# Kernel tuning notes

Hardware: AMD Instinct MI355X
Metric: run time of the kernel (lower is better)

Reference implementation:

```python
import math
import jax, jax.numpy as jnp
import numpy as np

B, T, M, S, D, H = 16, 512, 8, 32, 256, 4
HD = D // H


def setup_inputs() -> dict:
    key = jax.random.key(0)
    ks = jax.random.split(key, 16)
    w = 1.0 / math.sqrt(D)
    return {
        'q_temporal': jax.random.normal(ks[0], (B, T, M, D), jnp.float32),
        'q_static': jax.random.normal(ks[1], (B, S, D), jnp.float32),
        'k_temporal': jax.random.normal(ks[2], (B, T, M, D), jnp.float32),
        'v_temporal': jax.random.normal(ks[3], (B, T, M, D), jnp.float32),
        'k_static': jax.random.normal(ks[4], (B, S, D), jnp.float32),
        'v_static': jax.random.normal(ks[5], (B, S, D), jnp.float32),
        'q_w': jax.random.normal(ks[6], (D, D), jnp.float32) * w,
        'q_b': jax.random.normal(ks[7], (D,), jnp.float32) * w,
        'k_w': jax.random.normal(ks[8], (D, D), jnp.float32) * w,
        'k_b': jax.random.normal(ks[9], (D,), jnp.float32) * w,
        'v_w': jax.random.normal(ks[10], (D, D), jnp.float32) * w,
        'v_b': jax.random.normal(ks[11], (D,), jnp.float32) * w,
        'o_w': jax.random.normal(ks[12], (D, D), jnp.float32) * w,
        'o_b': jax.random.normal(ks[13], (D,), jnp.float32) * w,
        'mask_temporal': jax.random.randint(ks[14], (B, T, M), 0, 2).astype(jnp.int32),
        'mask_fcst': jax.random.randint(ks[15], (B, T, M), 0, 2).astype(jnp.int32),
        'mask_static': jnp.ones((B, S), jnp.int32),
    }


def _lin(x, w, b):
    # torch.nn.Linear: y = x @ W^T + b
    return x @ w.T + b


def reference(q_temporal, q_static, k_temporal, v_temporal, k_static, v_static,
              q_w, q_b, k_w, k_b, v_w, v_b, o_w, o_b,
              mask_temporal, mask_fcst, mask_static):
    scale = 1.0 / math.sqrt(HD)

    def heads5(x):  # [B,T,M,D] -> [B,H,T,M,HD]
        return x.reshape(B, T, M, H, HD).transpose(0, 3, 1, 2, 4)

    def heads3(x):  # [B,S,D] -> [B,H,S,HD]
        return x.reshape(B, -1, H, HD).transpose(0, 2, 1, 3)

    Qt = heads5(_lin(q_temporal, q_w, q_b))
    Kt = heads5(_lin(k_temporal, k_w, k_b))
    Vt = heads5(_lin(v_temporal, v_w, v_b))
    Qs = heads3(_lin(q_static, q_w, q_b))
    Ks = heads3(_lin(k_static, k_w, k_b))
    Vs = heads3(_lin(v_static, v_w, v_b))

    # additive masks: 0 where valid (==1), -inf where padded
    mt = jnp.where(mask_temporal == 1, 0.0, -jnp.inf).astype(Qt.dtype)  # [B,T,M]
    ms = jnp.where(mask_static == 1, 0.0, -jnp.inf).astype(Qt.dtype)    # [B,S]

    # ---- temporal query branch ----
    # temp_temp: per-timestep modality-vs-modality attention, column key mask
    Qt_Kt = jnp.einsum('bhtmd,bhtnd->bhtmn', Qt, Kt) * scale + mt[:, None, :, None, :]
    # temp_static: temporal queries vs static keys
    Qt_Ks = jnp.einsum('bhtmd,bhsd->bhtms', Qt, Ks) * scale + ms[:, None, None, None, :]
    tw = jax.nn.softmax(jnp.concatenate([Qt_Kt, Qt_Ks], axis=-1), axis=-1)  # [B,H,T,M,M+S]
    QKV_t = (jnp.einsum('bhtmn,bhtnd->bhtmd', tw[..., :M], Vt)
             + jnp.einsum('bhtms,bhsd->bhtmd', tw[..., M:], Vs))
    out_t = _lin(QKV_t.transpose(0, 2, 3, 1, 4).reshape(B, T, M, D), o_w, o_b)

    # ---- static query branch ----
    Ktf = Kt.reshape(B, H, T * M, HD)  # flatten (T,M) key axis
    Vtf = Vt.reshape(B, H, T * M, HD)
    Qs_Kt = jnp.einsum('bhqd,bhkd->bhqk', Qs, Ktf) * scale + mt.reshape(B, 1, 1, T * M)
    Qs_Ks = jnp.einsum('bhqd,bhsd->bhqs', Qs, Ks) * scale + ms[:, None, None, :]
    sw = jax.nn.softmax(jnp.concatenate([Qs_Kt, Qs_Ks], axis=-1), axis=-1)  # [B,H,S,T*M+S]
    QKV_s = (jnp.einsum('bhqk,bhkd->bhqd', sw[..., :T * M], Vtf)
             + jnp.einsum('bhqs,bhsd->bhqd', sw[..., T * M:], Vs))
    out_s = _lin(QKV_s.transpose(0, 2, 1, 3).reshape(B, S, D), o_w, o_b)

    return (out_t, out_s, tw, sw)
```

## Files before the change

### kernel.cpp

```cpp
#include <hip/hip_runtime.h>

#define B_   16
#define T_   512
#define M_   8
#define S_   32
#define D_   256
#define H_   4
#define HD_  64
#define TM_  4096
#define NKT  40
#define NKS  4128

typedef unsigned short u16;
typedef __attribute__((ext_vector_type(8))) short bf16x8;
typedef __attribute__((ext_vector_type(4))) float f32x4;

__device__ __forceinline__ u16 f2b(float f) {
    union { float f; unsigned u; } v; v.f = f;
    unsigned r = v.u + 0x7FFF + ((v.u >> 16) & 1);
    return (u16)(r >> 16);
}
__device__ __forceinline__ float blo(unsigned u) {
    union { unsigned i; float f; } v; v.i = u << 16; return v.f;
}
__device__ __forceinline__ float bhi(unsigned u) {
    union { unsigned i; float f; } v; v.i = u & 0xFFFF0000u; return v.f;
}
__device__ __forceinline__ float b2f(u16 u) {
    union { unsigned i; float f; } v; v.i = ((unsigned)u) << 16; return v.f;
}
__device__ __forceinline__ unsigned pack2(float lo, float hi) {
    return (unsigned)f2b(lo) | ((unsigned)f2b(hi) << 16);
}
__device__ __forceinline__ uint4 cvt8(float4 a, float4 b) {
    uint4 r;
    r.x = pack2(a.x, a.y); r.y = pack2(a.z, a.w);
    r.z = pack2(b.x, b.y); r.w = pack2(b.z, b.w);
    return r;
}

#define GLL16(g, l) __builtin_amdgcn_global_load_lds( \
    (const __attribute__((address_space(1))) void*)(g), \
    (__attribute__((address_space(3))) void*)(l), 16, 0, 0)

__global__ __launch_bounds__(256) void k_cvt_w(const float* __restrict__ W0,
                                               const float* __restrict__ W1,
                                               const float* __restrict__ W2,
                                               u16* __restrict__ dst)
{
    const int sel = blockIdx.y;
    const float* W = sel == 0 ? W0 : sel == 1 ? W1 : W2;
    u16* d = dst + sel * 65536;
    const int i0 = (blockIdx.x * 256 + threadIdx.x) * 8;
    const float4 a = *(const float4*)(W + i0);
    const float4 b = *(const float4*)(W + i0 + 4);
    *(uint4*)(d + i0) = cvt8(a, b);
}

template<int XBF, int OUTF32>
__global__ __launch_bounds__(256, 2) void k_gemm_db(
    const void* __restrict__ X0, const void* __restrict__ X1, const void* __restrict__ X2,
    const u16* __restrict__ Wb, int wstride,
    const float* __restrict__ b0, const float* __restrict__ b1, const float* __restrict__ b2,
    void* __restrict__ Y0, void* __restrict__ Y1, void* __restrict__ Y2)
{
    __shared__ __align__(16) u16 sA[20480];
    __shared__ __align__(16) u16 sB[16384];
    const int sel = blockIdx.y;
    const void*  Xv   = sel == 0 ? X0 : sel == 1 ? X1 : X2;
    const float* bias = sel == 0 ? b0 : sel == 1 ? b1 : b2;
    void*        Yv   = sel == 0 ? Y0 : sel == 1 ? Y1 : Y2;
    const u16* W = Wb + sel * wstride;
    const int tid = threadIdx.x;
    const size_t r0 = (size_t)blockIdx.x * 64;
    const int wave = tid >> 6, lane = tid & 63;
    const int c = lane & 15, g = lane >> 4;
    const int swzk = g ^ ((c >> 1) & 3);
    const int swzl = (lane & 3) ^ ((lane >> 3) & 3);

#define STAGE_B(k0, bi)                                                         \
    _Pragma("unroll")                                                           \
    for (int i = 0; i < 4; ++i) {                                               \
        const int row = i * 64 + wave * 16 + (lane >> 2);                       \
        GLL16(W + (size_t)row * 256 + (k0) + swzl * 8,                          \
              sB + (bi) * 8192 + (i * 256 + wave * 64) * 8);                    \
    }

    STAGE_B(0, 0)

    if (XBF) {
#pragma unroll
        for (int j = 0; j < 8; ++j) {
            const int row = j * 8 + wave * 2 + (lane >> 5);
            const uint4 v = *(const uint4*)((const u16*)Xv + (r0 + row) * 256
                                            + (lane & 31) * 8);
            *(uint4*)(sA + ((lane & 31) >> 2) * 2560 + row * 40 + (lane & 3) * 8) = v;
        }
    } else {
#pragma unroll
        for (int j = 0; j < 16; ++j) {
            const int row = j * 4 + wave;
            const float4 v = *(const float4*)((const float*)Xv + (r0 + row) * 256
                                              + lane * 4);
            uint2 p; p.x = pack2(v.x, v.y); p.y = pack2(v.z, v.w);
            *(uint2*)(sA + (lane >> 3) * 2560 + row * 40 + (lane & 7) * 4) = p;
        }
    }
    __syncthreads();

    f32x4 acc[4][4];
#pragma unroll
    for (int i = 0; i < 4; ++i)
#pragma unroll
        for (int j = 0; j < 4; ++j) acc[i][j] = (f32x4){0, 0, 0, 0};

#pragma unroll
    for (int k = 0; k < 8; ++k) {
        const int cur = k & 1;
        if (k < 7) { STAGE_B((k + 1) * 32, cur ^ 1) }
        bf16x8 a[4], b[4];
#pragma unroll
        for (int f = 0; f < 4; ++f)
            a[f] = *(const bf16x8*)(sA + k * 2560 + (f * 16 + c) * 40 + g * 8);
#pragma unroll
        for (int f = 0; f < 4; ++f)
            b[f] = *(const bf16x8*)(sB + cur * 8192
                                    + (wave * 64 + f * 16 + c) * 32 + swzk * 8);
#pragma unroll
        for (int rf = 0; rf < 4; ++rf)
#pragma unroll
            for (int cf = 0; cf < 4; ++cf)
                acc[rf][cf] = __builtin_amdgcn_mfma_f32_16x16x32_bf16(
                    a[rf], b[cf], acc[rf][cf], 0, 0, 0);
        if (k < 7) __syncthreads();
    }
#undef STAGE_B

    const int orow = g * 4, ocol = c;
    if (OUTF32) {
#pragma unroll
        for (int cf = 0; cf < 4; ++cf) {
            const int col = wave * 64 + cf * 16 + ocol;
            const float bv = bias[col];
#pragma unroll
            for (int rf = 0; rf < 4; ++rf)
#pragma unroll
                for (int r = 0; r < 4; ++r)
                    ((float*)Yv)[(r0 + rf * 16 + orow + r) * 256 + col] =
                        acc[rf][cf][r] + bv;
        }
    } else {
        __syncthreads();
#pragma unroll
        for (int cf = 0; cf < 4; ++cf) {
            const int col = wave * 64 + cf * 16 + ocol;
            const float bv = bias[col];
#pragma unroll
            for (int rf = 0; rf < 4; ++rf)
#pragma unroll
                for (int r = 0; r < 4; ++r)
                    sA[(rf * 16 + orow + r) * 264 + col] = f2b(acc[rf][cf][r] + bv);
        }
        __syncthreads();
#pragma unroll
        for (int i = 0; i < 8; ++i) {
            const int s = i * 256 + tid;
            const int row = s >> 5, seg = s & 31;
            *(uint4*)((u16*)Yv + (r0 + row) * 256 + seg * 8) =
                *(const uint4*)(sA + row * 264 + seg * 8);
        }
    }
}

__global__ __launch_bounds__(256) void k_attn_t(
    const u16* __restrict__ Qt, const u16* __restrict__ Kt, const u16* __restrict__ Vt,
    const u16* __restrict__ Ks, const u16* __restrict__ Vs,
    const int* __restrict__ maskT, const int* __restrict__ maskS,
    float* __restrict__ tw, u16* __restrict__ qkvt)
{
    const int tp = blockIdx.x, b = blockIdx.y;
    const int t0 = tp * 2;
    __shared__ __align__(16) u16 sQ [4 * 2 * 16 * 32];
    __shared__ __align__(16) u16 sKT[4 * 2 * 16 * 32];
    __shared__ __align__(16) u16 sKS[4 * 2 * 32 * 32];
    __shared__ __align__(16) u16 sVT[4 * 64 * 72];
    __shared__ __align__(16) u16 sP [4 * 16 * 72];
    __shared__ int smT[2][8];
    __shared__ int smS[32];
    const int tid = threadIdx.x;

#pragma unroll
    for (int i = 0; i < 2; ++i) {
        const int fl = tid + i * 256;
        const int r = fl >> 5, c32 = fl & 31;
        const int h = c32 >> 3, ks = (c32 >> 2) & 1, seg = c32 & 3;
        const size_t src = (((size_t)b * T_ + t0 + (r >> 3)) * 8 + (r & 7)) * 256 + c32 * 8;
        const int dst = h * 1024 + ks * 512 + r * 32 + seg * 8;
        *(uint4*)(sQ  + dst) = *(const uint4*)(Qt + src);
        *(uint4*)(sKT + dst) = *(const uint4*)(Kt + src);
    }
#pragma unroll
    for (int i = 0; i < 4; ++i) {
        const int fl = tid + i * 256;
        const int r = fl >> 5, c32 = fl & 31;
        const int h = c32 >> 3, ks = (c32 >> 2) & 1, seg = c32 & 3;
        *(uint4*)(sKS + h * 2048 + ks * 1024 + r * 32 + seg * 8) =
            *(const uint4*)(Ks + ((size_t)b * S_ + r) * 256 + c32 * 8);
    }
    {
        const int key = tid & 63, dg = tid >> 6;
        const u16* vrow = nullptr;
        if (key < 16)      vrow = Vt + (((size_t)b * T_ + t0 + (key >> 3)) * 8 + (key & 7)) * 256;
        else if (key < 48) vrow = Vs + ((size_t)b * S_ + (key - 16)) * 256;
#pragma unroll
        for (int i = 0; i < 8; ++i) {
            const int dseg = dg * 8 + i;
            uint4 v = {0, 0, 0, 0};
            if (vrow) v = *(const uint4*)(vrow + dseg * 8);
            const int h = dseg >> 3, dl0 = (dseg & 7) * 8;
            const u16* pv = (const u16*)&v;
#pragma unroll
            for (int j = 0; j < 8; ++j)
                sVT[h * 4608 + (dl0 + j) * 72 + key] = pv[j];
        }
    }
    if (tid < 16) smT[tid >> 3][tid & 7] =
        maskT[((size_t)b * T_ + t0 + (tid >> 3)) * 8 + (tid & 7)];
    if (tid < 32) smS[tid] = maskS[b * S_ + tid];
    __syncthreads();

    const int h = tid >> 6, lane = tid & 63;
    const int c = lane & 15, g = lane >> 4, th = g >> 1;

    f32x4 at = {0,0,0,0}, as0 = {0,0,0,0}, as1 = {0,0,0,0};
#pragma unroll
    for (int ks = 0; ks < 2; ++ks) {
        bf16x8 aq = *(const bf16x8*)(sQ  + h * 1024 + ks * 512 + c * 32 + g * 8);
        bf16x8 bt = *(const bf16x8*)(sKT + h * 1024 + ks * 512 + c * 32 + g * 8);
        bf16x8 b0 = *(const bf16x8*)(sKS + h * 2048 + ks * 1024 + c * 32 + g * 8);
        bf16x8 b1 = *(const bf16x8*)(sKS + h * 2048 + ks * 1024 + 512 + c * 32 + g * 8);
        at  = __builtin_amdgcn_mfma_f32_16x16x32_bf16(aq, bt, at, 0, 0, 0);
        as0 = __builtin_amdgcn_mfma_f32_16x16x32_bf16(aq, b0, as0, 0, 0, 0);
        as1 = __builtin_amdgcn_mfma_f32_16x16x32_bf16(aq, b1, as1, 0, 0, 0);
    }

    const int vt = ((c >> 3) == th) ? smT[th][c & 7] : 0;
    const int v0 = smS[c], v1 = smS[16 + c];
    float st[4], s0[4], s1[4], mx[4];
#pragma unroll
    for (int r = 0; r < 4; ++r) {
        st[r] = vt ? at[r]  * 0.125f : -1e30f;
        s0[r] = v0 ? as0[r] * 0.125f : -1e30f;
        s1[r] = v1 ? as1[r] * 0.125f : -1e30f;
        mx[r] = fmaxf(fmaxf(st[r], s0[r]), s1[r]);
    }
#pragma unroll
    for (int o = 1; o < 16; o <<= 1)
#pragma unroll
        for (int r = 0; r < 4; ++r) mx[r] = fmaxf(mx[r], __shfl_xor(mx[r], o));
    float pt[4], p0[4], p1[4], sum[4];
#pragma unroll
    for (int r = 0; r < 4; ++r) {
        pt[r] = __expf(st[r] - mx[r]);
        p0[r] = __expf(s0[r] - mx[r]);
        p1[r] = __expf(s1[r] - mx[r]);
        sum[r] = pt[r] + p0[r] + p1[r];
    }
#pragma unroll
    for (int o = 1; o < 16; o <<= 1)
#pragma unroll
        for (int r = 0; r < 4; ++r) sum[r] += __shfl_xor(sum[r], o);
#pragma unroll
    for (int r = 0; r < 4; ++r) {
        const float inv = 1.0f / sum[r];
        pt[r] *= inv; p0[r] *= inv; p1[r] *= inv;
    }

#pragma unroll
    for (int r = 0; r < 4; ++r) {
        const int row = g * 4 + r;
        const int tt = t0 + (row >> 3), m = row & 7;
        float* twp = tw + ((((size_t)b * H_ + h) * T_ + tt) * 8 + m) * NKT;
        if ((c >> 3) == th) twp[c & 7] = pt[r];
        twp[8 + c]  = p0[r];
        twp[24 + c] = p1[r];
        u16* sp = sP + h * 1152 + row * 72;
        sp[c]      = f2b(pt[r]);
        sp[16 + c] = f2b(p0[r]);
        sp[32 + c] = f2b(p1[r]);
        sp[48 + c] = 0;
    }

    f32x4 o4[4] = {{0,0,0,0}, {0,0,0,0}, {0,0,0,0}, {0,0,0,0}};
#pragma unroll
    for (int ks = 0; ks < 2; ++ks) {
        bf16x8 pa = *(const bf16x8*)(sP + h * 1152 + c * 72 + ks * 32 + g * 8);
#pragma unroll
        for (int dt = 0; dt < 4; ++dt) {
            bf16x8 pb = *(const bf16x8*)(sVT + h * 4608 + (dt * 16 + c) * 72 + ks * 32 + g * 8);
            o4[dt] = __builtin_amdgcn_mfma_f32_16x16x32_bf16(pa, pb, o4[dt], 0, 0, 0);
        }
    }
#pragma unroll
    for (int dt = 0; dt < 4; ++dt)
#pragma unroll
        for (int r = 0; r < 4; ++r) {
            const int row = g * 4 + r;
            const int tt = t0 + (row >> 3), m = row & 7;
            qkvt[(((size_t)b * T_ + tt) * 8 + m) * 256 + h * 64 + dt * 16 + c] = f2b(o4[dt][r]);
        }
}

__global__ __launch_bounds__(256) void k_attn_s_scores(
    const u16* __restrict__ Qs, const u16* __restrict__ Kt, const u16* __restrict__ Ks,
    const int* __restrict__ maskT, const int* __restrict__ maskS,
    float* __restrict__ raw)
{
    const int ch = blockIdx.x, h = blockIdx.y, b = blockIdx.z;
    const int nk = (ch < 32) ? 128 : 32;
    const int k0 = ch * 128;
    __shared__ __align__(16) u16 sQ[2 * 32 * 32];
    __shared__ __align__(16) u16 sK[2 * 128 * 32];
    __shared__ int sM[128];
    const int tid = threadIdx.x;

    {   const int q = tid >> 3, c8 = tid & 7;
        const int ks = c8 >> 2, seg = c8 & 3;
        *(uint4*)(sQ + ks * 1024 + q * 32 + seg * 8) =
            *(const uint4*)(Qs + ((size_t)b * S_ + q) * 256 + h * 64 + c8 * 8);
    }
#pragma unroll
    for (int i = 0; i < 4; ++i) {
        const int fl = tid + i * 256;
        const int key = fl >> 3, c8 = fl & 7;
        const int ks = c8 >> 2, seg = c8 & 3;
        if (key < nk) {
            const u16* src = (ch < 32)
                ? (Kt + ((size_t)b * TM_ + k0 + key) * 256 + h * 64 + c8 * 8)
                : (Ks + ((size_t)b * S_  +      key) * 256 + h * 64 + c8 * 8);
            *(uint4*)(sK + ks * 4096 + key * 32 + seg * 8) = *(const uint4*)src;
        }
    }
    if (tid < nk) sM[tid] = (ch < 32) ? maskT[(size_t)b * TM_ + k0 + tid]
                                      : maskS[b * S_ + tid];
    __syncthreads();

    const int w = tid >> 6, lane = tid & 63;
    if (w * 32 >= nk) return;
    const int c = lane & 15, g = lane >> 4;

    f32x4 acc[2][2] = {{{0,0,0,0}, {0,0,0,0}}, {{0,0,0,0}, {0,0,0,0}}};
#pragma unroll
    for (int ks = 0; ks < 2; ++ks) {
        bf16x8 a0 = *(const bf16x8*)(sQ + ks * 1024 +        c * 32 + g * 8);
        bf16x8 a1 = *(const bf16x8*)(sQ + ks * 1024 + 512 +  c * 32 + g * 8);
        bf16x8 b0 = *(const bf16x8*)(sK + ks * 4096 + (w * 32 +      c) * 32 + g * 8);
        bf16x8 b1 = *(const bf16x8*)(sK + ks * 4096 + (w * 32 + 16 + c) * 32 + g * 8);
        acc[0][0] = __builtin_amdgcn_mfma_f32_16x16x32_bf16(a0, b0, acc[0][0], 0, 0, 0);
        acc[0][1] = __builtin_amdgcn_mfma_f32_16x16x32_bf16(a0, b1, acc[0][1], 0, 0, 0);
        acc[1][0] = __builtin_amdgcn_mfma_f32_16x16x32_bf16(a1, b0, acc[1][0], 0, 0, 0);
        acc[1][1] = __builtin_amdgcn_mfma_f32_16x16x32_bf16(a1, b1, acc[1][1], 0, 0, 0);
    }
#pragma unroll
    for (int rt = 0; rt < 2; ++rt)
#pragma unroll
        for (int ct = 0; ct < 2; ++ct) {
            const int kl = w * 32 + ct * 16 + c;
            const float madd = sM[kl] ? 0.f : -1e30f;
#pragma unroll
            for (int r = 0; r < 4; ++r) {
                const int q = rt * 16 + g * 4 + r;
                raw[(((size_t)b * H_ + h) * S_ + q) * NKS + k0 + kl] =
                    acc[rt][ct][r] * 0.125f + madd;
            }
        }
}

__global__ __launch_bounds__(256) void k_attn_s_softmax(
    const float* __restrict__ raw, float* __restrict__ sw)
{
    const int q = blockIdx.x, h = blockIdx.y, b = blockIdx.z;
    __shared__ float sRow[NKS];
    __shared__ float red[8];
    const int tid = threadIdx.x;
    const size_t base = (((size_t)b * H_ + h) * S_ + q) * NKS;

    float mx = -1e30f;
    for (int i = tid; i < NKS; i += 256) {
        const float v = raw[base + i];
        sRow[i] = v;
        mx = fmaxf(mx, v);
    }
    for (int o = 32; o; o >>= 1) mx = fmaxf(mx, __shfl_xor(mx, o));
    if ((tid & 63) == 0) red[tid >> 6] = mx;
    __syncthreads();
    mx = fmaxf(fmaxf(red[0], red[1]), fmaxf(red[2], red[3]));

    float sum = 0.f;
    for (int i = tid; i < NKS; i += 256) {
        const float e = __expf(sRow[i] - mx);
        sRow[i] = e;
        sum += e;
    }
    for (int o = 32; o; o >>= 1) sum += __shfl_xor(sum, o);
    if ((tid & 63) == 0) red[4 + (tid >> 6)] = sum;
    __syncthreads();
    sum = (red[4] + red[5]) + (red[6] + red[7]);
    const float inv = 1.0f / sum;

    for (int i = tid; i < NKS; i += 256)
        sw[base + i] = sRow[i] * inv;
}

__global__ __launch_bounds__(256) void k_attn_s_pv_part(
    const float* __restrict__ w, const u16* __restrict__ Vt, const u16* __restrict__ Vs,
    float* __restrict__ part)
{
    const int ch = blockIdx.x, h = blockIdx.y, b = blockIdx.z;
    const int nk = (ch < 32) ? 128 : 32;
    const int k0 = ch * 128;
    __shared__ float sW[32][132];
    __shared__ __align__(16) u16 sV[128 * 64];
    const int tid = threadIdx.x;

#pragma unroll
    for (int i = 0; i < 4; ++i) {
        const int fl = tid + i * 256;
        const int q = fl >> 5, k4 = fl & 31;
        if (k4 * 4 < nk)
            *(float4*)&sW[q][k4 * 4] =
                *(const float4*)(w + (((size_t)b * H_ + h) * S_ + q) * NKS + k0 + k4 * 4);
    }
#pragma unroll
    for (int i = 0; i < 4; ++i) {
        const int fl = tid + i * 256;
        const int key = fl >> 3, pp = fl & 7;
        if (key < nk) {
            const u16* src = (ch < 32)
                ? (Vt + ((size_t)b * TM_ + k0 + key) * D_ + h * HD_ + pp * 8)
                : (Vs + ((size_t)b * S_  +      key) * D_ + h * HD_ + pp * 8);
            ((uint4*)sV)[fl] = *(const uint4*)src;
        }
    }
    __syncthreads();

    const int d = tid & 63, qg = tid >> 6;
    float acc[8] = {0,0,0,0,0,0,0,0};
    for (int kk = 0; kk < nk; kk += 4) {
        const float v0 = b2f(sV[(kk + 0) * 64 + d]);
        const float v1 = b2f(sV[(kk + 1) * 64 + d]);
        const float v2 = b2f(sV[(kk + 2) * 64 + d]);
        const float v3 = b2f(sV[(kk + 3) * 64 + d]);
#pragma unroll
        for (int j = 0; j < 8; ++j) {
            const float4 wv = *(const float4*)&sW[qg * 8 + j][kk];
            acc[j] += wv.x * v0 + wv.y * v1 + wv.z * v2 + wv.w * v3;
        }
    }

    float* pb = part + (((size_t)ch * B_ + b) * H_ + h) * 2048;
#pragma unroll
    for (int j = 0; j < 8; ++j)
        pb[(qg * 8 + j) * 64 + d] = acc[j];
}

__global__ __launch_bounds__(256) void k_attn_s_pv_red(
    const float* __restrict__ part, u16* __restrict__ qkvs)
{
    const int h = blockIdx.x, b = blockIdx.y;
    const int tid = threadIdx.x;
    for (int i = tid; i < 2048; i += 256) {
        float s = 0.f;
#pragma unroll
        for (int c = 0; c < 33; ++c)
            s += part[(((size_t)c * B_ + b) * H_ + h) * 2048 + i];
        const int q = i >> 6, d = i & 63;
        qkvs[((size_t)b * S_ + q) * D_ + h * HD_ + d] = f2b(s);
    }
}

extern "C" void kernel_launch(void* const* d_in, const int* in_sizes, int n_in,
                              void* d_out, int out_size, void* d_ws, size_t ws_size,
                              hipStream_t stream)
{
    const float* q_t = (const float*)d_in[0];
    const float* q_s = (const float*)d_in[1];
    const float* k_t = (const float*)d_in[2];
    const float* v_t = (const float*)d_in[3];
    const float* k_s = (const float*)d_in[4];
    const float* v_s = (const float*)d_in[5];
    const float* q_w = (const float*)d_in[6];
    const float* q_b = (const float*)d_in[7];
    const float* k_w = (const float*)d_in[8];
    const float* k_b = (const float*)d_in[9];
    const float* v_w = (const float*)d_in[10];
    const float* v_b = (const float*)d_in[11];
    const float* o_w = (const float*)d_in[12];
    const float* o_b = (const float*)d_in[13];
    const int* maskT = (const int*)d_in[14];
    const int* maskS = (const int*)d_in[16];
    float* out = (float*)d_out;

    char* ws = (char*)d_ws;
    u16*   Kt   = (u16*)(ws + 0);
    u16*   Vt   = (u16*)(ws + 33554432);
    u16*   QKVt = (u16*)(ws + 67108864);
    float* part = (float*)(ws + 67108864);
    u16*   Wqkv = (u16*)(ws + 67108864);
    u16*   Qs   = (u16*)(ws + 100663296);
    u16*   Ks   = (u16*)(ws + 100925440);
    u16*   Vs   = (u16*)(ws + 101187584);
    u16*   QKVs = (u16*)(ws + 101449728);
    u16*   Qt   = (u16*)(ws + 101711872);
    float* raw  = (float*)(ws + 101711872);
    u16*   Wo   = (u16*)(ws + 101711872);
    if (ws_size < 135528448) return;

    float* out_t = out;
    float* out_s = out + 16777216;
    float* tw    = out + 16908288;
    float* sw    = out + 27394048;

    const dim3 blk(256);
    k_cvt_w<<<dim3(32, 3), blk, 0, stream>>>(q_w, k_w, v_w, Wqkv);

    k_gemm_db<0, 0><<<dim3(1024, 3), blk, 0, stream>>>(
        q_t, k_t, v_t, Wqkv, 65536, q_b, k_b, v_b, Qt, Kt, Vt);
    k_gemm_db<0, 0><<<dim3(8, 3), blk, 0, stream>>>(
        q_s, k_s, v_s, Wqkv, 65536, q_b, k_b, v_b, Qs, Ks, Vs);

    k_attn_t<<<dim3(256, 16), blk, 0, stream>>>(Qt, Kt, Vt, Ks, Vs, maskT, maskS, tw, QKVt);

    k_cvt_w<<<dim3(32, 1), blk, 0, stream>>>(o_w, o_w, o_w, Wo);
    k_gemm_db<1, 1><<<dim3(1024, 1), blk, 0, stream>>>(
        QKVt, QKVt, QKVt, Wo, 0, o_b, o_b, o_b, out_t, out_t, out_t);

    k_attn_s_scores<<<dim3(33, 4, 16), blk, 0, stream>>>(Qs, Kt, Ks, maskT, maskS, raw);
    k_attn_s_softmax<<<dim3(32, 4, 16), blk, 0, stream>>>(raw, sw);
    k_cvt_w<<<dim3(32, 1), blk, 0, stream>>>(o_w, o_w, o_w, Wo);
    k_attn_s_pv_part<<<dim3(33, 4, 16), blk, 0, stream>>>(sw, Vt, Vs, part);
    k_attn_s_pv_red<<<dim3(4, 16), blk, 0, stream>>>(part, QKVs);

    k_gemm_db<1, 1><<<dim3(8, 1), blk, 0, stream>>>(
        QKVs, QKVs, QKVs, Wo, 0, o_b, o_b, o_b, out_s, out_s, out_s);
}
```

Baseline: 263.3 us.

## Split GEMM output columns across blocks and double-buffer A tile for occupancy

The projection GEMM now gives each block a 64x128 output tile instead of 64x256, which doubles the grid and shrinks shared memory from about 72KB to about 26KB. Launch bounds are raised so up to six blocks can share a CU. The A tile is no longer loaded whole up front; it is double-buffered per 32-wide k-step, with global loads issued before the MFMAs and the LDS write done after them. The aim is better latency hiding through occupancy and overlap, at the cost of reading the activation rows twice (once per column half) and fewer accumulators per wave.

```diff
diff --git a/kernel.cpp b/kernel.cpp
--- a/kernel.cpp
+++ b/kernel.cpp
@@ -58,89 +58,97 @@
 }
 
 template<int XBF, int OUTF32>
-__global__ __launch_bounds__(256, 2) void k_gemm_db(
+__global__ __launch_bounds__(256, 6) void k_gemm_n(
     const void* __restrict__ X0, const void* __restrict__ X1, const void* __restrict__ X2,
     const u16* __restrict__ Wb, int wstride,
     const float* __restrict__ b0, const float* __restrict__ b1, const float* __restrict__ b2,
     void* __restrict__ Y0, void* __restrict__ Y1, void* __restrict__ Y2)
 {
-    __shared__ __align__(16) u16 sA[20480];
-    __shared__ __align__(16) u16 sB[16384];
+    __shared__ __align__(16) u16 smem[13312];
+    u16* sA = smem;
+    u16* sB = smem + 5120;
     const int sel = blockIdx.y;
     const void*  Xv   = sel == 0 ? X0 : sel == 1 ? X1 : X2;
     const float* bias = sel == 0 ? b0 : sel == 1 ? b1 : b2;
     void*        Yv   = sel == 0 ? Y0 : sel == 1 ? Y1 : Y2;
-    const u16* W = Wb + sel * wstride;
+    const int ch = blockIdx.x & 1;
+    const size_t r0 = (size_t)(blockIdx.x >> 1) * 64;
+    const u16* W = Wb + (size_t)sel * wstride + ch * 128 * 256;
     const int tid = threadIdx.x;
-    const size_t r0 = (size_t)blockIdx.x * 64;
     const int wave = tid >> 6, lane = tid & 63;
     const int c = lane & 15, g = lane >> 4;
     const int swzk = g ^ ((c >> 1) & 3);
     const int swzl = (lane & 3) ^ ((lane >> 3) & 3);
-
+    const int arow = tid >> 2, aseg = tid & 3;
+
+    f32x4 acc[4][2];
+#pragma unroll
+    for (int i = 0; i < 4; ++i)
+#pragma unroll
+        for (int j = 0; j < 2; ++j) acc[i][j] = (f32x4){0, 0, 0, 0};
+
+    float4 fa[2];
+    uint4  ua;
+
+#define LOAD_A(k0)                                                              \
+    if (XBF) {                                                                  \
+        ua = *(const uint4*)((const u16*)Xv + (r0 + arow) * 256 + (k0) + aseg * 8); \
+    } else {                                                                    \
+        const float* gA = (const float*)Xv + (r0 + arow) * 256 + (k0) + aseg * 8; \
+        fa[0] = *(const float4*)gA; fa[1] = *(const float4*)(gA + 4);           \
+    }
+#define WRITE_A(bi)                                                             \
+    {   u16* d = sA + (bi) * 2560 + arow * 40 + aseg * 8;                       \
+        if (XBF) *(uint4*)d = ua;                                               \
+        else     *(uint4*)d = cvt8(fa[0], fa[1]);                               \
+    }
 #define STAGE_B(k0, bi)                                                         \
     _Pragma("unroll")                                                           \
-    for (int i = 0; i < 4; ++i) {                                               \
+    for (int i = 0; i < 2; ++i) {                                               \
         const int row = i * 64 + wave * 16 + (lane >> 2);                       \
         GLL16(W + (size_t)row * 256 + (k0) + swzl * 8,                          \
-              sB + (bi) * 8192 + (i * 256 + wave * 64) * 8);                    \
-    }
-
-    STAGE_B(0, 0)
-
-    if (XBF) {
-#pragma unroll
-        for (int j = 0; j < 8; ++j) {
-            const int row = j * 8 + wave * 2 + (lane >> 5);
-            const uint4 v = *(const uint4*)((const u16*)Xv + (r0 + row) * 256
-                                            + (lane & 31) * 8);
-            *(uint4*)(sA + ((lane & 31) >> 2) * 2560 + row * 40 + (lane & 3) * 8) = v;
-        }
-    } else {
-#pragma unroll
-        for (int j = 0; j < 16; ++j) {
-            const int row = j * 4 + wave;
-            const float4 v = *(const float4*)((const float*)Xv + (r0 + row) * 256
-                                              + lane * 4);
-            uint2 p; p.x = pack2(v.x, v.y); p.y = pack2(v.z, v.w);
-            *(uint2*)(sA + (lane >> 3) * 2560 + row * 40 + (lane & 7) * 4) = p;
-        }
-    }
-    __syncthreads();
-
-    f32x4 acc[4][4];
-#pragma unroll
-    for (int i = 0; i < 4; ++i)
-#pragma unroll
-        for (int j = 0; j < 4; ++j) acc[i][j] = (f32x4){0, 0, 0, 0};
+              sB + (bi) * 4096 + (i * 256 + wave * 64) * 8);                    \
+    }
+
+    {
+        LOAD_A(0)
+        WRITE_A(0)
+        STAGE_B(0, 0)
+    }
 
 #pragma unroll
     for (int k = 0; k < 8; ++k) {
         const int cur = k & 1;
-        if (k < 7) { STAGE_B((k + 1) * 32, cur ^ 1) }
-        bf16x8 a[4], b[4];
+        __syncthreads();
+        if (k < 7) {
+            LOAD_A((k + 1) * 32)
+            STAGE_B((k + 1) * 32, cur ^ 1)
+        }
+        bf16x8 a[4], b[2];
 #pragma unroll
         for (int f = 0; f < 4; ++f)
-            a[f] = *(const bf16x8*)(sA + k * 2560 + (f * 16 + c) * 40 + g * 8);
-#pragma unroll
-        for (int f = 0; f < 4; ++f)
-            b[f] = *(const bf16x8*)(sB + cur * 8192
-                                    + (wave * 64 + f * 16 + c) * 32 + swzk * 8);
+            a[f] = *(const bf16x8*)(sA + cur * 2560 + (f * 16 + c) * 40 + g * 8);
+#pragma unroll
+        for (int f = 0; f < 2; ++f)
+            b[f] = *(const bf16x8*)(sB + cur * 4096
+                                    + (wave * 32 + f * 16 + c) * 32 + swzk * 8);
 #pragma unroll
         for (int rf = 0; rf < 4; ++rf)
 #pragma unroll
-            for (int cf = 0; cf < 4; ++cf)
+            for (int cf = 0; cf < 2; ++cf)
                 acc[rf][cf] = __builtin_amdgcn_mfma_f32_16x16x32_bf16(
                     a[rf], b[cf], acc[rf][cf], 0, 0, 0);
-        if (k < 7) __syncthreads();
-    }
+        if (k < 7) WRITE_A(cur ^ 1)
+    }
+#undef LOAD_A
+#undef WRITE_A
 #undef STAGE_B
 
     const int orow = g * 4, ocol = c;
     if (OUTF32) {
 #pragma unroll
-        for (int cf = 0; cf < 4; ++cf) {
-            const int col = wave * 64 + cf * 16 + ocol;
+        for (int cf = 0; cf < 2; ++cf) {
+            const int col = ch * 128 + wave * 32 + cf * 16 + ocol;
             const float bv = bias[col];
 #pragma unroll
             for (int rf = 0; rf < 4; ++rf)
@@ -152,22 +160,22 @@
     } else {
         __syncthreads();
 #pragma unroll
-        for (int cf = 0; cf < 4; ++cf) {
-            const int col = wave * 64 + cf * 16 + ocol;
-            const float bv = bias[col];
+        for (int cf = 0; cf < 2; ++cf) {
+            const int wloc = wave * 32 + cf * 16 + ocol;
+            const float bv = bias[ch * 128 + wloc];
 #pragma unroll
             for (int rf = 0; rf < 4; ++rf)
 #pragma unroll
                 for (int r = 0; r < 4; ++r)
-                    sA[(rf * 16 + orow + r) * 264 + col] = f2b(acc[rf][cf][r] + bv);
+                    smem[(rf * 16 + orow + r) * 136 + wloc] = f2b(acc[rf][cf][r] + bv);
         }
         __syncthreads();
 #pragma unroll
-        for (int i = 0; i < 8; ++i) {
+        for (int i = 0; i < 4; ++i) {
             const int s = i * 256 + tid;
-            const int row = s >> 5, seg = s & 31;
-            *(uint4*)((u16*)Yv + (r0 + row) * 256 + seg * 8) =
-                *(const uint4*)(sA + row * 264 + seg * 8);
+            const int row = s >> 4, seg = s & 15;
+            *(uint4*)((u16*)Yv + (r0 + row) * 256 + ch * 128 + seg * 8) =
+                *(const uint4*)(smem + row * 136 + seg * 8);
         }
     }
 }
@@ -524,15 +532,15 @@
     const dim3 blk(256);
     k_cvt_w<<<dim3(32, 3), blk, 0, stream>>>(q_w, k_w, v_w, Wqkv);
 
-    k_gemm_db<0, 0><<<dim3(1024, 3), blk, 0, stream>>>(
+    k_gemm_n<0, 0><<<dim3(2048, 3), blk, 0, stream>>>(
         q_t, k_t, v_t, Wqkv, 65536, q_b, k_b, v_b, Qt, Kt, Vt);
-    k_gemm_db<0, 0><<<dim3(8, 3), blk, 0, stream>>>(
+    k_gemm_n<0, 0><<<dim3(16, 3), blk, 0, stream>>>(
         q_s, k_s, v_s, Wqkv, 65536, q_b, k_b, v_b, Qs, Ks, Vs);
 
     k_attn_t<<<dim3(256, 16), blk, 0, stream>>>(Qt, Kt, Vt, Ks, Vs, maskT, maskS, tw, QKVt);
 
     k_cvt_w<<<dim3(32, 1), blk, 0, stream>>>(o_w, o_w, o_w, Wo);
-    k_gemm_db<1, 1><<<dim3(1024, 1), blk, 0, stream>>>(
+    k_gemm_n<1, 1><<<dim3(2048, 1), blk, 0, stream>>>(
         QKVt, QKVt, QKVt, Wo, 0, o_b, o_b, o_b, out_t, out_t, out_t);
 
     k_attn_s_scores<<<dim3(33, 4, 16), blk, 0, stream>>>(Qs, Kt, Ks, maskT, maskS, raw);
@@ -541,6 +549,6 @@
     k_attn_s_pv_part<<<dim3(33, 4, 16), blk, 0, stream>>>(sw, Vt, Vs, part);
     k_attn_s_pv_red<<<dim3(4, 16), blk, 0, stream>>>(part, QKVs);
 
-    k_gemm_db<1, 1><<<dim3(8, 1), blk, 0, stream>>>(
+    k_gemm_n<1, 1><<<dim3(16, 1), blk, 0, stream>>>(
         QKVs, QKVs, QKVs, Wo, 0, o_b, o_b, o_b, out_s, out_s, out_s);
 }
```

Result: no change. 268.1 us (+1.8%).
